# Optimization experiments

Measured on AMD Instinct MI355X. Metric: run time of the kernel, lower is better.

## Reference

```python
import jax, jax.numpy as jnp
import numpy as np

T, B, I, H = 32, 16, 512, 512
OFF = 441  # triu diagonal offset from get_sparse_config(512,512,0.99) -> 2556 coeffs


def _idct_weight(N):
    # Ortho DCT-II matrix C[k,n]; the idct DCTLayer weight is C^T so that
    # linear(x) = x @ (C^T)^T = x @ C = idct_ortho(x).
    n = np.arange(N)
    C = np.sqrt(2.0 / N) * np.cos(np.pi * (2 * n[None, :] + 1) * n[:, None] / (2 * N))
    C[0] /= np.sqrt(2.0)
    return jnp.asarray(C.T, dtype=jnp.float32)


def setup_inputs() -> dict:
    key = jax.random.key(0)
    ks = jax.random.split(key, 8)
    rows_np, cols_np = np.triu_indices(H, OFF, I)
    NC = rows_np.shape[0]  # 2556

    def u(k, shape, fan):
        s = 1.0 / np.sqrt(fan)
        return jax.random.uniform(k, shape, jnp.float32, -s, s)

    return {
        "input_": jax.random.normal(ks[0], (T, B, I), jnp.float32),
        # coefficient-generating LSTMs (torch nn.LSTM(input_dim, n_coeffs)),
        # b = b_ih + b_hh folded into one bias (mathematically identical)
        "wih_ih": u(ks[1], (4 * NC, I), NC),
        "wih_hh": u(ks[2], (4 * NC, NC), NC),
        "wih_b": u(ks[3], (4 * NC,), NC),
        "whh_ih": u(ks[4], (4 * NC, I), NC),
        "whh_hh": u(ks[5], (4 * NC, NC), NC),
        "whh_b": u(ks[6], (4 * NC,), NC),
        "coef_scaler_ih": jnp.ones((NC,), jnp.float32),
        "coef_scaler_hh": jnp.ones((NC,), jnp.float32),
        "bias": u(ks[7], (H,), H),
        "idct_in": _idct_weight(I),
        "idct_hid": _idct_weight(H),
        "rows": jnp.asarray(rows_np, jnp.int32),
        "cols": jnp.asarray(cols_np, jnp.int32),
    }


def _lstm(x_seq, Wih, Whh, b):
    # Standard torch LSTM, gate order i,f,g,o. x_seq: [T,B,in]
    C = Whh.shape[-1]

    def step(carry, x):
        h, c = carry
        g = x @ Wih.T + h @ Whh.T + b
        i, f, gg, o = jnp.split(g, 4, axis=-1)
        c = jax.nn.sigmoid(f) * c + jax.nn.sigmoid(i) * jnp.tanh(gg)
        h = jax.nn.sigmoid(o) * jnp.tanh(c)
        return (h, c), h

    h0 = jnp.zeros((x_seq.shape[1], C), x_seq.dtype)
    _, hs = jax.lax.scan(step, (h0, h0), x_seq)
    return hs  # [T,B,C]


def _reconstruct(coeffs, rows, cols, A, Bm, out_dim, in_dim):
    # scatter sparse DCT coeffs into upper-diagonal band, flip left-right,
    # then 2D inverse DCT via two dense matmuls: W = Bm @ fliplr(S) @ A^T
    S = jnp.zeros((coeffs.shape[0], out_dim, in_dim), coeffs.dtype)
    S = S.at[:, rows, cols].set(coeffs)
    Sf = S[:, :, ::-1]
    return jnp.einsum('hk,bki,ji->bhj', Bm, Sf, A)  # [b,out_dim,in_dim]


def _forward(input_, wih_ih, wih_hh, wih_b, whh_ih, whh_hh, whh_b,
             coef_scaler_ih, coef_scaler_hh, bias, idct_in, idct_hid, rows, cols):
    coeffs_ih = _lstm(input_, wih_ih, wih_hh, wih_b) * coef_scaler_ih  # [T,B,NC]
    coeffs_hh = _lstm(input_, whh_ih, whh_hh, whh_b) * coef_scaler_hh

    def step(h, inp):
        x, cih, chh = inp
        Wih = _reconstruct(cih, rows, cols, idct_in, idct_hid, H, I)   # [B,H,I]
        Whh = _reconstruct(chh, rows, cols, idct_hid, idct_hid, H, H)  # [B,H,H]
        h = jnp.tanh(jnp.einsum('bi,bhi->bh', x, Wih)
                     + jnp.einsum('bj,bhj->bh', h, Whh) + bias)
        return h, h

    h0 = jnp.zeros((input_.shape[1], H), input_.dtype)
    _, out = jax.lax.scan(step, h0, (input_, coeffs_ih, coeffs_hh))
    return out  # [T,B,H]


def reference(input_, wih_ih, wih_hh, wih_b, whh_ih, whh_hh, whh_b,
              coef_scaler_ih, coef_scaler_hh, bias, idct_in, idct_hid, rows, cols):
    return _forward(input_, wih_ih, wih_hh, wih_b, whh_ih, whh_hh, whh_b,
                    coef_scaler_ih, coef_scaler_hh, bias, idct_in, idct_hid, rows, cols)
```

## Files before the change

kernel.cpp:

```cpp
#include <hip/hip_runtime.h>
#include <hip/hip_bf16.h>

#define T_ 32
#define B_ 16
#define I_ 512
#define H_ 512
#define OFF_ 441
#define NR_ 71
#define NC_ 2556
#define G4_ (4*NC_)
#define NCP_ 2560
#define NPR_ 10240
#define NTIL_ 640

typedef __attribute__((ext_vector_type(8))) short bf16x8;
typedef __attribute__((ext_vector_type(4))) float f32x4;
typedef __attribute__((ext_vector_type(4))) int   i32x4;

__device__ __forceinline__ ushort bfc(float f) {
    __hip_bfloat16 h = __float2bfloat16(f);
    return *(ushort*)&h;
}
__device__ __forceinline__ float b2f(ushort u) {
    return __uint_as_float((uint)u << 16);
}
__device__ __forceinline__ float sigf(float x) { return 1.f / (1.f + expf(-x)); }

__global__ void k_zero(float* __restrict__ p, int n) {
    int i = blockIdx.x * 256 + threadIdx.x;
    if (i < n) p[i] = 0.f;
}

__global__ void k_cvt_x(const float* __restrict__ x, ushort* __restrict__ xb) {
    int i = blockIdx.x * 256 + threadIdx.x;
    float4 v = ((const float4*)x)[i];
    ushort4 o; o.x = bfc(v.x); o.y = bfc(v.y); o.z = bfc(v.z); o.w = bfc(v.w);
    ((ushort4*)xb)[i] = o;
}

__global__ void k_cvt_w512p(const float* __restrict__ W0, const float* __restrict__ W1,
                            ushort* __restrict__ dst) {
    int l = blockIdx.z;
    const float* src = l ? W1 : W0;
    size_t idx = (size_t)blockIdx.x * 256 + threadIdx.x;
    int np = (int)(idx >> 7), kq = (int)(idx & 127);
    ushort4 o; o.x = 0; o.y = 0; o.z = 0; o.w = 0;
    int jc = np >> 2, q = np & 3;
    if (jc < NC_) {
        float4 v = *(const float4*)(src + ((size_t)q * NC_ + jc) * I_ + kq * 4);
        o.x = bfc(v.x); o.y = bfc(v.y); o.z = bfc(v.z); o.w = bfc(v.w);
    }
    ((ushort4*)(dst + ((size_t)l * NPR_ + np) * I_))[kq] = o;
}

__global__ __launch_bounds__(256) void k_cvt_whh_i8(const float* __restrict__ W0,
        const float* __restrict__ W1,
        signed char* __restrict__ dst, float* __restrict__ sW) {
    const int l = blockIdx.z;
    const float* src = l ? W1 : W0;
    const int np = blockIdx.x * 4 + (threadIdx.x >> 6);
    const int lane = threadIdx.x & 63;
    const int jc = np >> 2, q = np & 3;
    float w[40];
    float mx = 0.f;
    if (jc < NC_) {
        const float* row = src + ((size_t)q * NC_ + jc) * NC_;
        #pragma unroll
        for (int g = 0; g < 5; ++g) {
            int k0 = g * 512 + lane * 8;
            #pragma unroll
            for (int e = 0; e < 8; ++e) {
                int k = k0 + e;
                float v = (k < NC_) ? row[k] : 0.f;
                w[g * 8 + e] = v;
                mx = fmaxf(mx, fabsf(v));
            }
        }
    } else {
        #pragma unroll
        for (int i = 0; i < 40; ++i) w[i] = 0.f;
    }
    #pragma unroll
    for (int d = 1; d < 64; d <<= 1) mx = fmaxf(mx, __shfl_xor(mx, d));
    const float inv = (mx > 0.f) ? 127.f / mx : 0.f;
    const int nt = np >> 4, r = np & 15;
    signed char* obase = dst + (((size_t)l * NTIL_ + nt) * 40) * 1024;
    #pragma unroll
    for (int g = 0; g < 5; ++g) {
        int k0 = g * 512 + lane * 8;
        int ks = k0 >> 6, kgrp = (k0 >> 4) & 3, e = k0 & 15;
        uint lo = 0, hi = 0;
        #pragma unroll
        for (int ee = 0; ee < 4; ++ee) {
            lo |= ((uint)(uchar)(signed char)(int)rintf(w[g * 8 + ee] * inv)) << (8 * ee);
            hi |= ((uint)(uchar)(signed char)(int)rintf(w[g * 8 + 4 + ee] * inv)) << (8 * ee);
        }
        *(uint2*)(obase + (size_t)ks * 1024 + (kgrp * 16 + r) * 16 + e) = make_uint2(lo, hi);
    }
    if (lane == 0) sW[(size_t)l * NPR_ + np] = (mx > 0.f) ? mx / 127.f : 0.f;
}

__global__ __launch_bounds__(256) void k_gih_mfma(const ushort* __restrict__ Xbf,
        const ushort* __restrict__ Wp,
        const float* __restrict__ b0, const float* __restrict__ b1,
        ushort* __restrict__ preT) {
    const int l = blockIdx.z;
    const float* bb = l ? b1 : b0;
    const int wid = threadIdx.x >> 6, lane = threadIdx.x & 63;
    const int nt = blockIdx.x * 4 + wid;
    __shared__ ushort lds_a[32 * 64 * 8];
    const int srow = lane & 15, skq = (lane >> 4) * 8;
    const ushort* wp = Wp + ((size_t)l * NPR_ + nt * 16 + srow) * I_ + skq;
    f32x4 acc[32];
    #pragma unroll
    for (int mt = 0; mt < 32; ++mt) acc[mt] = (f32x4){0.f, 0.f, 0.f, 0.f};
    for (int ks = 0; ks < 16; ++ks) {
        #pragma unroll
        for (int i = 0; i < 8; ++i) {
            int mt = wid * 8 + i;
            bf16x8 xv = *(const bf16x8*)(Xbf + (size_t)(mt * 16 + srow) * I_ + ks * 32 + skq);
            *(bf16x8*)(lds_a + (mt * 64 + lane) * 8) = xv;
        }
        bf16x8 b = *(const bf16x8*)(wp + ks * 32);
        __syncthreads();
        #pragma unroll
        for (int mt = 0; mt < 32; ++mt) {
            bf16x8 a = *(const bf16x8*)(lds_a + (mt * 64 + lane) * 8);
            acc[mt] = __builtin_amdgcn_mfma_f32_16x16x32_bf16(a, b, acc[mt], 0, 0, 0);
        }
        __syncthreads();
    }
    const int n = nt * 16 + srow;
    const float bv = (n < G4_) ? bb[(size_t)(n & 3) * NC_ + (n >> 2)] : 0.f;
    const int r0 = (lane >> 4) * 4;
    ushort* po = preT + ((size_t)l * NPR_ + n) * 512;
    #pragma unroll
    for (int mt = 0; mt < 32; ++mt) {
        ushort4 o;
        o.x = bfc(acc[mt][0] + bv); o.y = bfc(acc[mt][1] + bv);
        o.z = bfc(acc[mt][2] + bv); o.w = bfc(acc[mt][3] + bv);
        *(ushort4*)(po + mt * 16 + r0) = o;
    }
}

__global__ __launch_bounds__(256, 4) void k_step(const signed char* __restrict__ Wq8,
        const float* __restrict__ sW, const ushort* __restrict__ preT,
        const signed char* __restrict__ h_in, signed char* __restrict__ h_out,
        float* __restrict__ cst, float* __restrict__ hbuf,
        const float* __restrict__ scal_ih, const float* __restrict__ scal_hh,
        int t) {
    const int l = blockIdx.z;
    const int nt0 = blockIdx.x * 4;
    const int tid = threadIdx.x;
    const int w = tid >> 6, lane = tid & 63;
    float pv[4], swv[4];
    const int item_g = tid >> 6;
    const int b_g = tid & 15, jq_g = (tid >> 4) & 3;
    const int nt_g = nt0 + item_g;
    const int jc_g = nt_g * 4 + jq_g;
    {
        #pragma unroll
        for (int q = 0; q < 4; ++q) {
            const int row = nt_g * 16 + jq_g * 4 + q;
            pv[q]  = b2f(preT[((size_t)l * NPR_ + row) * 512 + t * 16 + b_g]);
            swv[q] = sW[(size_t)l * NPR_ + row] * (1.f / 127.f);
        }
    }
    const signed char* wbase = Wq8 + (((size_t)l * NTIL_ + nt0) * 40 + w * 10) * 1024 + lane * 16;
    const signed char* hbase = h_in + (size_t)l * 81920 + (w * 10) * 1024 + lane * 16;
    i32x4 sh[4], sl[4];
    #pragma unroll
    for (int i = 0; i < 4; ++i) { sh[i] = (i32x4){0,0,0,0}; sl[i] = (i32x4){0,0,0,0}; }
    #pragma unroll 2
    for (int ks = 0; ks < 10; ++ks) {
        i32x4 ah = *(const i32x4*)(hbase + ks * 1024);
        i32x4 al = *(const i32x4*)(hbase + 40960 + ks * 1024);
        #pragma unroll
        for (int i = 0; i < 4; ++i) {
            i32x4 bw = *(const i32x4*)(wbase + (size_t)i * 40960 + ks * 1024);
            sh[i] = __builtin_amdgcn_mfma_i32_16x16x64_i8(ah, bw, sh[i], 0, 0, 0);
            sl[i] = __builtin_amdgcn_mfma_i32_16x16x64_i8(al, bw, sl[i], 0, 0, 0);
        }
    }
    __shared__ float gl[4][4][16][17];
    const int col = lane & 15;
    const int m0 = (lane >> 4) * 4;
    #pragma unroll
    for (int i = 0; i < 4; ++i)
        #pragma unroll
        for (int v = 0; v < 4; ++v)
            gl[i][w][col][m0 + v] = (float)sh[i][v] + (float)sl[i][v] * (1.f / 127.f);
    __syncthreads();
    if (jc_g < NC_) {
        float g[4];
        #pragma unroll
        for (int q = 0; q < 4; ++q) {
            float s = gl[item_g][0][jq_g * 4 + q][b_g] + gl[item_g][1][jq_g * 4 + q][b_g]
                    + gl[item_g][2][jq_g * 4 + q][b_g] + gl[item_g][3][jq_g * 4 + q][b_g];
            g[q] = s * swv[q] + pv[q];
        }
        float* cp = cst + ((size_t)l * NC_ + jc_g) * B_ + b_g;
        float ci = *cp;
        float cn = sigf(g[1]) * ci + sigf(g[0]) * tanhf(g[2]);
        float hn = sigf(g[3]) * tanhf(cn);
        *cp = cn;
        const int ks = jc_g >> 6, kgrp = (jc_g >> 4) & 3, e = jc_g & 15;
        const size_t off = (size_t)l * 81920 + (size_t)ks * 1024 + (kgrp * 16 + b_g) * 16 + e;
        float t1 = hn * 127.f;
        float fhi = rintf(t1);
        float flo = rintf((t1 - fhi) * 127.f);
        h_out[off]         = (signed char)(int)fhi;
        h_out[off + 40960] = (signed char)(int)flo;
        float sc = (l ? scal_hh : scal_ih)[jc_g];
        hbuf[(((size_t)l * T_ + t) * B_ + b_g) * NC_ + jc_g] = hn * sc;
    }
}

__global__ void k_bt(const float* __restrict__ Bh, float* __restrict__ Bt) {
    int idx = blockIdx.x * 256 + threadIdx.x;
    if (idx < NR_ * H_) {
        int k = idx / H_, h = idx - k * H_;
        Bt[idx] = Bh[(size_t)h * H_ + k];
    }
}

__global__ void k_at(const float* __restrict__ Ain, float* __restrict__ AinT) {
    int idx = blockIdx.x * 256 + threadIdx.x;
    if (idx < NR_ * I_) {
        int g = idx / I_, j = idx - g * I_;
        AinT[idx] = Ain[(size_t)j * I_ + g];
    }
}

__global__ __launch_bounds__(576) void k_yih(const float* __restrict__ x,
        const float* __restrict__ AinT, const float* __restrict__ Bt,
        const float* __restrict__ hbuf0, float* __restrict__ yih) {
    __shared__ __align__(16) float xl[I_];
    __shared__ float u[NR_ + 1];
    __shared__ __align__(16) float v[NR_ + 1];
    const int tb = blockIdx.x, tid = threadIdx.x;
    for (int i = tid; i < I_; i += 576) xl[i] = x[(size_t)tb * I_ + i];
    if (tid == 0) { u[NR_] = 0.f; v[NR_] = 0.f; }
    const int g = tid >> 3, lane = tid & 7;
    __syncthreads();
    if (g < NR_) {
        const float* ap = AinT + (size_t)g * I_ + lane * 4;
        const float* hp = xl + lane * 4;
        float a = 0.f;
        #pragma unroll
        for (int m = 0; m < 16; ++m) {
            float4 aq = *(const float4*)(ap + m * 32);
            float4 hq = *(const float4*)(hp + m * 32);
            a += aq.x * hq.x + aq.y * hq.y + aq.z * hq.z + aq.w * hq.w;
        }
        a += __shfl_xor(a, 1); a += __shfl_xor(a, 2); a += __shfl_xor(a, 4);
        if (lane == 0) u[g] = a;
    }
    __syncthreads();
    if (g < NR_) {
        int start = g * NR_ - (g * (g - 1)) / 2;
        int cnt = NR_ - g;
        const float* cf = hbuf0 + (size_t)tb * NC_ + start;
        float a = 0.f;
        for (int m = lane; m < cnt; m += 8) a += cf[m] * u[cnt - 1 - m];
        a += __shfl_xor(a, 1); a += __shfl_xor(a, 2); a += __shfl_xor(a, 4);
        if (lane == 0) v[g] = a;
    }
    __syncthreads();
    if (tid < H_) {
        float4 vv[18];
        #pragma unroll
        for (int q = 0; q < 18; ++q) vv[q] = *(const float4*)(v + q * 4);
        float a0 = 0.f, a1 = 0.f;
        #pragma unroll
        for (int k = 0; k < NR_; ++k) {
            float vk = ((const float*)vv)[k];
            ((k & 1) ? a1 : a0) += Bt[(size_t)k * H_ + tid] * vk;
        }
        yih[(size_t)tb * H_ + tid] = a0 + a1;
    }
}

#define BTP_ 520
__global__ __launch_bounds__(576) void k_seq(const float* __restrict__ yih,
        const float* __restrict__ Bt, const float* __restrict__ cf_all,
        const float* __restrict__ bias, float* __restrict__ out) {
    __shared__ __align__(16) float bt[NR_ * BTP_];
    __shared__ __align__(16) float hl[2][H_];
    __shared__ float u[NR_ + 1];
    __shared__ __align__(16) float v[NR_ + 1];
    const int b = blockIdx.x, tid = threadIdx.x;
    for (int i = tid; i < NR_ * H_; i += 576)
        bt[(i >> 9) * BTP_ + (i & 511)] = Bt[i];
    for (int i = tid; i < H_; i += 576) hl[0][i] = 0.f;
    if (tid == 0) { u[NR_] = 0.f; v[NR_] = 0.f; }
    const float bv = (tid < H_) ? bias[tid] : 0.f;
    const int g = tid >> 3, lane = tid & 7;
    int start = 0, cnt = 0;
    if (g < NR_) { start = g * NR_ - (g * (g - 1)) / 2; cnt = NR_ - g; }
    int p = 0;
    __syncthreads();
    for (int t = 0; t < T_; ++t) {
        float yv = 0.f;
        if (tid < H_) yv = yih[((size_t)t * B_ + b) * H_ + tid];
        float cfv[9];
        if (g < NR_) {
            const float* cf = cf_all + ((size_t)t * B_ + b) * NC_ + start;
            #pragma unroll
            for (int mi = 0; mi < 9; ++mi) {
                int m = mi * 8 + lane;
                cfv[mi] = cf[m < cnt ? m : (cnt - 1)];
            }
        }
        if (g < NR_) {
            const float* bp = bt + g * BTP_ + lane * 4;
            const float* hp = hl[p] + lane * 4;
            float a = 0.f;
            #pragma unroll
            for (int m = 0; m < 16; ++m) {
                float4 bq = *(const float4*)(bp + m * 32);
                float4 hq = *(const float4*)(hp + m * 32);
                a += bq.x * hq.x + bq.y * hq.y + bq.z * hq.z + bq.w * hq.w;
            }
            a += __shfl_xor(a, 1); a += __shfl_xor(a, 2); a += __shfl_xor(a, 4);
            if (lane == 0) u[g] = a;
        }
        __syncthreads();
        if (g < NR_) {
            float a = 0.f;
            #pragma unroll
            for (int mi = 0; mi < 9; ++mi) {
                int m = mi * 8 + lane;
                a += (m < cnt) ? cfv[mi] * u[cnt - 1 - m] : 0.f;
            }
            a += __shfl_xor(a, 1); a += __shfl_xor(a, 2); a += __shfl_xor(a, 4);
            if (lane == 0) v[g] = a;
        }
        __syncthreads();
        if (tid < H_) {
            float4 vv[18];
            #pragma unroll
            for (int q = 0; q < 18; ++q) vv[q] = *(const float4*)(v + q * 4);
            float a0 = 0.f, a1 = 0.f;
            #pragma unroll
            for (int k = 0; k < NR_; ++k) {
                float vk = ((const float*)vv)[k];
                ((k & 1) ? a1 : a0) += bt[k * BTP_ + tid] * vk;
            }
            float hv = tanhf(yv + a0 + a1 + bv);
            out[((size_t)t * B_ + b) * H_ + tid] = hv;
            hl[p ^ 1][tid] = hv;
        }
        __syncthreads();
        p ^= 1;
    }
}

extern "C" void kernel_launch(void* const* d_in, const int* in_sizes, int n_in,
                              void* d_out, int out_size, void* d_ws, size_t ws_size,
                              hipStream_t stream) {
    const float* x        = (const float*)d_in[0];
    const float* wih_ih   = (const float*)d_in[1];
    const float* wih_hh   = (const float*)d_in[2];
    const float* wih_b    = (const float*)d_in[3];
    const float* whh_ih   = (const float*)d_in[4];
    const float* whh_hh   = (const float*)d_in[5];
    const float* whh_b    = (const float*)d_in[6];
    const float* scal_ih  = (const float*)d_in[7];
    const float* scal_hh  = (const float*)d_in[8];
    const float* bias     = (const float*)d_in[9];
    const float* idct_in  = (const float*)d_in[10];
    const float* idct_hid = (const float*)d_in[11];
    float* out = (float*)d_out;

    const size_t WP8_B  = (size_t)2 * NPR_ * NCP_;
    const size_t SW_B   = (size_t)2 * NPR_ * 4;
    const size_t PRET_B = (size_t)2 * NPR_ * 512 * 2;
    const size_t HBUF_B = (size_t)2 * T_ * B_ * NC_ * 4;
    const size_t HBF_B  = (size_t)2 * 2 * 2 * 40960;
    const size_t CST_B  = (size_t)2 * NC_ * B_ * 4;
    const size_t YIH_B  = (size_t)T_ * B_ * H_ * 4;
    const size_t BT_B   = (size_t)NR_ * H_ * 4;
    const size_t AT_B   = (size_t)NR_ * I_ * 4;
    const size_t need = WP8_B + SW_B + PRET_B + HBUF_B + HBF_B + CST_B + YIH_B + BT_B + AT_B + 4096;

    char* ws = (char*)d_ws;
    size_t off = 0;
    auto alloc = [&](size_t bytes) -> void* {
        void* p = (void*)(ws + off);
        off += (bytes + 255) & ~(size_t)255;
        return p;
    };

    if (ws_size < need) return;

    signed char* Wp8 = (signed char*)alloc(WP8_B);
    float*  sW   = (float*)alloc(SW_B);
    ushort* preT = (ushort*)alloc(PRET_B);
    float*  hbuf = (float*)alloc(HBUF_B);
    signed char* hbf = (signed char*)alloc(HBF_B);
    float*  cst  = (float*)alloc(CST_B);
    float*  yih  = (float*)alloc(YIH_B);
    float*  Bt   = (float*)alloc(BT_B);
    float*  AinT = (float*)alloc(AT_B);
    ushort* Wih_p = (ushort*)Wp8;
    ushort* Xbf   = (ushort*)((char*)Wp8 + 21000192);

    {
        int n = (int)((HBF_B + CST_B) / 4);
        hipLaunchKernelGGL(k_zero, dim3((n + 255) / 256), dim3(256), 0, stream,
                           (float*)hbf, n);
    }
    hipLaunchKernelGGL(k_cvt_x, dim3(256), dim3(256), 0, stream, x, Xbf);
    hipLaunchKernelGGL(k_cvt_w512p, dim3(NPR_ * 128 / 256, 1, 2), dim3(256), 0, stream,
                       wih_ih, whh_ih, Wih_p);
    hipLaunchKernelGGL(k_gih_mfma, dim3(160, 1, 2), dim3(256), 0, stream,
                       Xbf, Wih_p, wih_b, whh_b, preT);
    hipLaunchKernelGGL(k_cvt_whh_i8, dim3(NPR_ / 4, 1, 2), dim3(256), 0, stream,
                       wih_hh, whh_hh, Wp8, sW);

    const size_t HS = (size_t)2 * 81920;
    for (int t = 0; t < T_; ++t) {
        const signed char* hin  = hbf + (size_t)(t & 1) * HS;
        signed char*       hout = hbf + (size_t)((t & 1) ^ 1) * HS;
        hipLaunchKernelGGL(k_step, dim3(NTIL_ / 4, 1, 2), dim3(256), 0, stream,
                           Wp8, sW, preT, hin, hout, cst, hbuf, scal_ih, scal_hh, t);
    }

    hipLaunchKernelGGL(k_bt, dim3((NR_ * H_ + 255) / 256), dim3(256), 0, stream,
                       idct_hid, Bt);
    hipLaunchKernelGGL(k_at, dim3((NR_ * I_ + 255) / 256), dim3(256), 0, stream,
                       idct_in, AinT);
    hipLaunchKernelGGL(k_yih, dim3(T_ * B_), dim3(576), 0, stream,
                       x, AinT, Bt, hbuf, yih);
    hipLaunchKernelGGL(k_seq, dim3(B_), dim3(576), 0, stream,
                       yih, Bt, hbuf + (size_t)T_ * B_ * NC_, bias, out);
}
```

Baseline: 662.2 us.

## Pre-swizzle input-projection operands into MFMA fragment layout and drop LDS staging

The bf16 conversion kernels for X and the input-to-hidden weights now write data directly in the per-lane MFMA fragment order, so each lane loads contiguous 16-byte fragments. The input-projection GEMM drops its LDS staging and the two barriers per k-step, reading A fragments straight from global memory. The M dimension is split across a new grid y axis, which halves the accumulator count and doubles the block count. The trade-off is that X fragments are reloaded by many waves through cache instead of being shared through LDS. This only affects the preprocessing GEMM, not the recurrent step loop.

```diff
diff --git a/kernel.cpp b/kernel.cpp
--- a/kernel.cpp
+++ b/kernel.cpp
@@ -31,26 +31,42 @@
     if (i < n) p[i] = 0.f;
 }
 
-__global__ void k_cvt_x(const float* __restrict__ x, ushort* __restrict__ xb) {
-    int i = blockIdx.x * 256 + threadIdx.x;
-    float4 v = ((const float4*)x)[i];
-    ushort4 o; o.x = bfc(v.x); o.y = bfc(v.y); o.z = bfc(v.z); o.w = bfc(v.w);
-    ((ushort4*)xb)[i] = o;
-}
-
-__global__ void k_cvt_w512p(const float* __restrict__ W0, const float* __restrict__ W1,
+__global__ void k_cvt_xq(const float* __restrict__ x, ushort* __restrict__ Xq) {
+    int tid = blockIdx.x * 256 + threadIdx.x;
+    int mt = tid >> 10, rem = tid & 1023;
+    int ks = rem >> 6, lane = rem & 63;
+    int row = lane & 15, kq = lane >> 4;
+    const float* src = x + ((size_t)(mt * 16 + row)) * I_ + ks * 32 + kq * 8;
+    float4 v0 = *(const float4*)(src);
+    float4 v1 = *(const float4*)(src + 4);
+    union { bf16x8 v; ushort us[8]; } o;
+    o.us[0] = bfc(v0.x); o.us[1] = bfc(v0.y); o.us[2] = bfc(v0.z); o.us[3] = bfc(v0.w);
+    o.us[4] = bfc(v1.x); o.us[5] = bfc(v1.y); o.us[6] = bfc(v1.z); o.us[7] = bfc(v1.w);
+    *(bf16x8*)(Xq + (size_t)tid * 8) = o.v;
+}
+
+__global__ void k_cvt_w512q(const float* __restrict__ W0, const float* __restrict__ W1,
                             ushort* __restrict__ dst) {
-    int l = blockIdx.z;
+    const int l = blockIdx.z;
     const float* src = l ? W1 : W0;
-    size_t idx = (size_t)blockIdx.x * 256 + threadIdx.x;
-    int np = (int)(idx >> 7), kq = (int)(idx & 127);
-    ushort4 o; o.x = 0; o.y = 0; o.z = 0; o.w = 0;
+    int tid = blockIdx.x * 256 + threadIdx.x;
+    int nt = tid >> 10, rem = tid & 1023;
+    int ks = rem >> 6, lane = rem & 63;
+    int row = lane & 15, kq = lane >> 4;
+    int np = nt * 16 + row;
     int jc = np >> 2, q = np & 3;
+    union { bf16x8 v; ushort us[8]; } o;
     if (jc < NC_) {
-        float4 v = *(const float4*)(src + ((size_t)q * NC_ + jc) * I_ + kq * 4);
-        o.x = bfc(v.x); o.y = bfc(v.y); o.z = bfc(v.z); o.w = bfc(v.w);
-    }
-    ((ushort4*)(dst + ((size_t)l * NPR_ + np) * I_))[kq] = o;
+        const float* sp = src + ((size_t)q * NC_ + jc) * I_ + ks * 32 + kq * 8;
+        float4 v0 = *(const float4*)(sp);
+        float4 v1 = *(const float4*)(sp + 4);
+        o.us[0] = bfc(v0.x); o.us[1] = bfc(v0.y); o.us[2] = bfc(v0.z); o.us[3] = bfc(v0.w);
+        o.us[4] = bfc(v1.x); o.us[5] = bfc(v1.y); o.us[6] = bfc(v1.z); o.us[7] = bfc(v1.w);
+    } else {
+        #pragma unroll
+        for (int e = 0; e < 8; ++e) o.us[e] = 0;
+    }
+    *(bf16x8*)(dst + ((size_t)l * NTIL_ * 1024 + tid) * 8) = o.v;
 }
 
 __global__ __launch_bounds__(256) void k_cvt_whh_i8(const float* __restrict__ W0,
@@ -100,46 +116,38 @@
     if (lane == 0) sW[(size_t)l * NPR_ + np] = (mx > 0.f) ? mx / 127.f : 0.f;
 }
 
-__global__ __launch_bounds__(256) void k_gih_mfma(const ushort* __restrict__ Xbf,
-        const ushort* __restrict__ Wp,
+__global__ __launch_bounds__(256) void k_gih_mfma(const ushort* __restrict__ Xq,
+        const ushort* __restrict__ Wq,
         const float* __restrict__ b0, const float* __restrict__ b1,
         ushort* __restrict__ preT) {
     const int l = blockIdx.z;
+    const int my = blockIdx.y;
     const float* bb = l ? b1 : b0;
     const int wid = threadIdx.x >> 6, lane = threadIdx.x & 63;
     const int nt = blockIdx.x * 4 + wid;
-    __shared__ ushort lds_a[32 * 64 * 8];
-    const int srow = lane & 15, skq = (lane >> 4) * 8;
-    const ushort* wp = Wp + ((size_t)l * NPR_ + nt * 16 + srow) * I_ + skq;
-    f32x4 acc[32];
-    #pragma unroll
-    for (int mt = 0; mt < 32; ++mt) acc[mt] = (f32x4){0.f, 0.f, 0.f, 0.f};
+    const ushort* wp = Wq + (((size_t)l * NTIL_ + nt) * 1024 + lane) * 8;
+    const ushort* xp = Xq + ((size_t)my * 16 * 1024 + lane) * 8;
+    f32x4 acc[16];
+    #pragma unroll
+    for (int i = 0; i < 16; ++i) acc[i] = (f32x4){0.f, 0.f, 0.f, 0.f};
     for (int ks = 0; ks < 16; ++ks) {
-        #pragma unroll
-        for (int i = 0; i < 8; ++i) {
-            int mt = wid * 8 + i;
-            bf16x8 xv = *(const bf16x8*)(Xbf + (size_t)(mt * 16 + srow) * I_ + ks * 32 + skq);
-            *(bf16x8*)(lds_a + (mt * 64 + lane) * 8) = xv;
-        }
-        bf16x8 b = *(const bf16x8*)(wp + ks * 32);
-        __syncthreads();
-        #pragma unroll
-        for (int mt = 0; mt < 32; ++mt) {
-            bf16x8 a = *(const bf16x8*)(lds_a + (mt * 64 + lane) * 8);
-            acc[mt] = __builtin_amdgcn_mfma_f32_16x16x32_bf16(a, b, acc[mt], 0, 0, 0);
-        }
-        __syncthreads();
-    }
-    const int n = nt * 16 + srow;
+        bf16x8 b = *(const bf16x8*)(wp + (size_t)ks * 512);
+        #pragma unroll
+        for (int i = 0; i < 16; ++i) {
+            bf16x8 a = *(const bf16x8*)(xp + ((size_t)i * 16 + ks) * 512);
+            acc[i] = __builtin_amdgcn_mfma_f32_16x16x32_bf16(a, b, acc[i], 0, 0, 0);
+        }
+    }
+    const int n = nt * 16 + (lane & 15);
     const float bv = (n < G4_) ? bb[(size_t)(n & 3) * NC_ + (n >> 2)] : 0.f;
     const int r0 = (lane >> 4) * 4;
-    ushort* po = preT + ((size_t)l * NPR_ + n) * 512;
-    #pragma unroll
-    for (int mt = 0; mt < 32; ++mt) {
+    ushort* po = preT + ((size_t)l * NPR_ + n) * 512 + my * 256;
+    #pragma unroll
+    for (int i = 0; i < 16; ++i) {
         ushort4 o;
-        o.x = bfc(acc[mt][0] + bv); o.y = bfc(acc[mt][1] + bv);
-        o.z = bfc(acc[mt][2] + bv); o.w = bfc(acc[mt][3] + bv);
-        *(ushort4*)(po + mt * 16 + r0) = o;
+        o.x = bfc(acc[i][0] + bv); o.y = bfc(acc[i][1] + bv);
+        o.z = bfc(acc[i][2] + bv); o.w = bfc(acc[i][3] + bv);
+        *(ushort4*)(po + i * 16 + r0) = o;
     }
 }
 
@@ -403,19 +411,19 @@
     float*  yih  = (float*)alloc(YIH_B);
     float*  Bt   = (float*)alloc(BT_B);
     float*  AinT = (float*)alloc(AT_B);
-    ushort* Wih_p = (ushort*)Wp8;
-    ushort* Xbf   = (ushort*)((char*)Wp8 + 21000192);
+    ushort* Wq   = (ushort*)Wp8;
+    ushort* Xq   = (ushort*)((char*)Wp8 + 21000192);
 
     {
         int n = (int)((HBF_B + CST_B) / 4);
         hipLaunchKernelGGL(k_zero, dim3((n + 255) / 256), dim3(256), 0, stream,
                            (float*)hbf, n);
     }
-    hipLaunchKernelGGL(k_cvt_x, dim3(256), dim3(256), 0, stream, x, Xbf);
-    hipLaunchKernelGGL(k_cvt_w512p, dim3(NPR_ * 128 / 256, 1, 2), dim3(256), 0, stream,
-                       wih_ih, whh_ih, Wih_p);
-    hipLaunchKernelGGL(k_gih_mfma, dim3(160, 1, 2), dim3(256), 0, stream,
-                       Xbf, Wih_p, wih_b, whh_b, preT);
+    hipLaunchKernelGGL(k_cvt_xq, dim3(128), dim3(256), 0, stream, x, Xq);
+    hipLaunchKernelGGL(k_cvt_w512q, dim3(2560, 1, 2), dim3(256), 0, stream,
+                       wih_ih, whh_ih, Wq);
+    hipLaunchKernelGGL(k_gih_mfma, dim3(160, 2, 2), dim3(256), 0, stream,
+                       Xq, Wq, wih_b, whh_b, preT);
     hipLaunchKernelGGL(k_cvt_whh_i8, dim3(NPR_ / 4, 1, 2), dim3(256), 0, stream,
                        wih_hh, whh_hh, Wp8, sW);
 
```

Measured after the change: 591.0 us. 10.7% less time.
